# Optimization experiments

Measured on AMD Instinct MI355X. Metric: run time of the kernel, lower is better.

## Reference

```python
import jax, jax.numpy as jnp
import numpy as np

C = 1.0          # ball curvature (Manifold default)
EPS = 1e-7
MIN_NORM = 1e-15

def _artanh(x):
    return jnp.arctanh(jnp.clip(x, -1.0 + EPS, 1.0 - EPS))

def _expmap0(u):
    # exp map at origin of the Poincare ball
    n = jnp.clip(jnp.linalg.norm(u, axis=-1, keepdims=True), MIN_NORM, None)
    sc = np.sqrt(C).astype(np.float32)
    return jnp.tanh(sc * n) * u / (sc * n)

def _mobius_add(x, y):
    x2 = jnp.sum(x * x, axis=-1, keepdims=True)
    y2 = jnp.sum(y * y, axis=-1, keepdims=True)
    xy = jnp.sum(x * y, axis=-1, keepdims=True)
    num = (1.0 + 2.0 * C * xy + C * y2) * x + (1.0 - C * x2) * y
    den = 1.0 + 2.0 * C * xy + C * C * x2 * y2
    return num / jnp.clip(den, MIN_NORM, None)

def setup_inputs() -> dict:
    key = jax.random.key(0)
    k1, k2, k3, k4 = jax.random.split(key, 4)
    N, D, U = 8192, 256, 128
    features = jax.random.normal(k1, (N, D), jnp.float32) * 0.1
    adj = jax.random.randint(k2, (N, N), 0, 2, jnp.int32)
    kernel = jax.random.normal(k3, (D, U), jnp.float32) * (1.0 / np.sqrt(D)).astype(np.float32)
    bias = jax.random.normal(k4, (U,), jnp.float32) * 0.01
    return {"features": features, "adj": adj, "kernel": kernel, "bias": bias}

def reference(features, adj, kernel, bias):
    sc = np.sqrt(C).astype(np.float32)
    # dense matmul then lift to the ball
    x = _expmap0(features @ kernel)                     # [N, U]
    # pairwise hyperbolic distance via closed form of ||mobius_add(-x_i, x_j)||
    x2 = jnp.sum(x * x, axis=-1)                        # [N]
    xy = x @ x.T                                        # [N, N]
    A = 1.0 - 2.0 * C * xy + C * x2[None, :]            # [N, N]
    B = (1.0 - C * x2)[:, None]                         # [N, 1]
    num_sq = A * A * x2[:, None] - 2.0 * A * B * xy + B * B * x2[None, :]
    den = 1.0 - 2.0 * C * xy + C * C * x2[:, None] * x2[None, :]
    mnorm = jnp.sqrt(jnp.clip(num_sq, 0.0, None)) / jnp.clip(den, MIN_NORM, None)
    dist = (2.0 / sc) * _artanh(sc * mnorm)             # sqdist ** 0.5 == distance, [N, N]
    # adjacency-masked softmax (zeros -> -inf, as in tf.where(a != 0, a, float.min))
    a = dist * adj.astype(dist.dtype)
    a = jnp.where(a != 0, a, jnp.finfo(a.dtype).min)
    att = jax.nn.softmax(a, axis=-1)                    # [N, N]
    # mobius_matvec with exchange=True: hyperbolic analogue of att @ x (row-wise norm rescale)
    mx = att @ x                                        # [N, U]
    x_n = jnp.clip(jnp.sqrt(x2)[:, None], MIN_NORM, None)
    mx_n = jnp.clip(jnp.linalg.norm(mx, axis=-1, keepdims=True), MIN_NORM, None)
    out = jnp.tanh(mx_n / x_n * _artanh(sc * x_n)) * mx / (sc * mx_n)
    # hyperbolic bias
    b = _expmap0(bias[None, :])                         # [1, U]
    return _mobius_add(out, b)
```

## Files before the change

### kernel.cpp

```cpp
#include <hip/hip_runtime.h>
#include <hip/hip_bf16.h>
#include <math.h>

#define Nn 8192
#define Dd 256
#define Uu 128
#define MI 16
#define NJC 8
#define JCL (Nn / NJC)
#define NIT (JCL / 16)

typedef __attribute__((ext_vector_type(4))) float f32x4;
typedef __attribute__((ext_vector_type(8))) short s16x8;
typedef __attribute__((ext_vector_type(4))) short s16x4;

#define MFMA_K32(a, b, c) __builtin_amdgcn_mfma_f32_16x16x32_bf16((a), (b), (c), 0, 0, 0)

#define GL_LDS(src, dst)                                                              \
  __builtin_amdgcn_global_load_lds(                                                   \
      (const __attribute__((address_space(1))) unsigned int*)(src),                   \
      (__attribute__((address_space(3))) unsigned int*)(dst), 16, 0, 0)

__device__ __forceinline__ f32x4 mfma_k16(s16x4 a, s16x4 b, f32x4 c){
#if __has_builtin(__builtin_amdgcn_mfma_f32_16x16x16bf16_1k)
  return __builtin_amdgcn_mfma_f32_16x16x16bf16_1k(a, b, c, 0, 0, 0);
#else
  asm("v_mfma_f32_16x16x16_bf16 %0, %1, %2, %0" : "+v"(c) : "v"(a), "v"(b));
  return c;
#endif
}

__device__ __forceinline__ short f2bf(float f){
  unsigned int u = __float_as_uint(f);
  u += 0x7fffu + ((u >> 16) & 1u);
  return (short)(u >> 16);
}

__device__ __forceinline__ float waveSum(float v){
  #pragma unroll
  for (int off = 32; off >= 1; off >>= 1) v += __shfl_xor(v, off);
  return v;
}

__global__ __launch_bounds__(128) void k_prep(const float* __restrict__ feat,
                                              const float* __restrict__ kern,
                                              short* __restrict__ xh,
                                              float* __restrict__ x2){
  const int t = threadIdx.x;
  const int n0 = blockIdx.x * 16;
  __shared__ float fS[16][Dd];
  __shared__ float red[2][16];
  {
    const f32x4* fg = (const f32x4*)(feat + (size_t)n0 * Dd);
    f32x4* fd = (f32x4*)fS;
    #pragma unroll
    for (int c = 0; c < 8; ++c) fd[c * 128 + t] = fg[c * 128 + t];
  }
  __syncthreads();
  float zz[16];
  #pragma unroll
  for (int r = 0; r < 16; ++r) zz[r] = 0.f;
  for (int dq = 0; dq < 64; ++dq){
    const int d = dq * 4;
    const float k0 = kern[(size_t)(d + 0) * Uu + t];
    const float k1 = kern[(size_t)(d + 1) * Uu + t];
    const float k2 = kern[(size_t)(d + 2) * Uu + t];
    const float k3 = kern[(size_t)(d + 3) * Uu + t];
    #pragma unroll
    for (int r = 0; r < 16; ++r){
      const f32x4 f4 = *(const f32x4*)&fS[r][d];
      zz[r] = fmaf(f4.x, k0, fmaf(f4.y, k1, fmaf(f4.z, k2, fmaf(f4.w, k3, zz[r]))));
    }
  }
  #pragma unroll
  for (int r = 0; r < 16; ++r){
    float v = waveSum(zz[r] * zz[r]);
    if ((t & 63) == 0) red[t >> 6][r] = v;
  }
  __syncthreads();
  #pragma unroll
  for (int r = 0; r < 16; ++r){
    const float ns  = red[0][r] + red[1][r];
    const float nrm = fmaxf(sqrtf(ns), 1e-15f);
    const float th  = tanhf(nrm);
    xh[(size_t)(n0 + r) * Uu + t] = f2bf(zz[r] * (th / nrm));
  }
  if (t < 16){
    const float ns  = red[0][t] + red[1][t];
    const float nrm = fmaxf(sqrtf(ns), 1e-15f);
    const float th  = tanhf(nrm);
    x2[n0 + t] = th * th;
  }
}

__global__ __launch_bounds__(256) void k_tr(const short* __restrict__ xh,
                                            short* __restrict__ v3){
  const int n0 = (blockIdx.x & 127) * 64;
  const int u0 = (blockIdx.x >> 7) * 64;
  __shared__ short tS[64][72];
  const int r  = threadIdx.x >> 2;
  const int c0 = (threadIdx.x & 3) * 16;
  const short* src = xh + (size_t)(n0 + r) * Uu + u0 + c0;
  *(s16x8*)&tS[r][c0]     = *(const s16x8*)(src);
  *(s16x8*)&tS[r][c0 + 8] = *(const s16x8*)(src + 8);
  __syncthreads();
  s16x8 b0, b1;
  #pragma unroll
  for (int k = 0; k < 8; ++k){ b0[k] = tS[c0 + k][r]; b1[k] = tS[c0 + 8 + k][r]; }
  short* dst = v3 + (size_t)((n0 + c0) >> 4) * (Uu * 16) + (size_t)(u0 + r) * 16;
  *(s16x8*)(dst)     = b0;
  *(s16x8*)(dst + 8) = b1;
}

__global__ __launch_bounds__(128) void k_bias(const float* __restrict__ bias,
                                              float* __restrict__ bb){
  const int t = threadIdx.x;
  __shared__ float red[2];
  float bv = bias[t];
  float v = waveSum(bv * bv);
  if ((t & 63) == 0) red[t >> 6] = v;
  __syncthreads();
  float n2  = red[0] + red[1];
  float nrm = fmaxf(sqrtf(n2), 1e-15f);
  float th  = tanhf(nrm);
  bb[t] = bv * th / nrm;
  if (t == 0) bb[Uu] = th * th;
}

__global__ __launch_bounds__(256, 4) void k_attn(const int* __restrict__ adj,
                                                 const short* __restrict__ xh,
                                                 const short* __restrict__ v3,
                                                 const float* __restrict__ x2g,
                                                 float* __restrict__ Opart,
                                                 float* __restrict__ lpart){
  const int t    = threadIdx.x;
  const int lane = t & 63;
  const int wid  = t >> 6;
  const int l15  = lane & 15;
  const int q4   = lane >> 4;
  const int ig   = blockIdx.x >> 3;
  const int jc   = blockIdx.x & 7;
  const int i0   = ig * 64 + wid * 16;
  const int irow = i0 + l15;
  const int jbase = jc * JCL;

  __shared__ short kb[2][2048];
  __shared__ short vb[2][2048];

  const char* ksrc = (const char*)xh + (size_t)jbase * 256
                     + (size_t)(lane & 15) * 256 + wid * 64 + (lane >> 4) * 16;
  const char* vsrc = (const char*)v3 + (size_t)jbase * 256 + wid * 1024 + lane * 16;

  GL_LDS(ksrc, (char*)&kb[0][0] + wid * 1024);
  GL_LDS(vsrc, (char*)&vb[0][0] + wid * 1024);

  s16x8 qf[4];
  {
    const short* qp = xh + (size_t)irow * Uu + q4 * 8;
    #pragma unroll
    for (int kk = 0; kk < 4; ++kk) qf[kk] = *(const s16x8*)(qp + kk * 32);
  }
  const float x2i  = x2g[irow];
  const float Bv   = 1.f - x2i;
  const float Bv2j = Bv * Bv;
  const float nBv2 = -2.f * Bv;

  f32x4 oc[8];
  #pragma unroll
  for (int uc = 0; uc < 8; ++uc) oc[uc] = (f32x4){0.f, 0.f, 0.f, 0.f};
  float lacc = 0.f;

  const int itDiag = ((i0 >> 10) == jc) ? ((i0 & 1023) >> 4) : -1;

  const int*   ap  = adj + (size_t)irow * Nn + jbase + q4 * 4;
  const float* x2p = x2g + jbase + q4 * 4;

  int4 aqC = *(const int4*)(ap);
  int4 aqN = *(const int4*)(ap + 16);

  asm volatile("s_waitcnt vmcnt(0)" ::: "memory");
  __builtin_amdgcn_s_barrier();
  __builtin_amdgcn_sched_barrier(0);

  #pragma unroll 1
  for (int it = 0; it < NIT; ++it){
    const int cur = it & 1;
    if (it + 1 < NIT){
      GL_LDS(ksrc + (size_t)(it + 1) * 4096, (char*)&kb[cur ^ 1][0] + wid * 1024);
      GL_LDS(vsrc + (size_t)(it + 1) * 4096, (char*)&vb[cur ^ 1][0] + wid * 1024);
    }
    __builtin_amdgcn_sched_barrier(0);
    const int4 aq2 = *(const int4*)(ap + (((it < NIT - 2) ? (it + 2) : (NIT - 1)) << 4));
    const f32x4 x2j = *(const f32x4*)(x2p + it * 16);

    s16x8 kf[4];
    #pragma unroll
    for (int kk = 0; kk < 4; ++kk)
      kf[kk] = *(const s16x8*)((const char*)&kb[cur][0] + kk * 1024 + lane * 16);
    s16x4 vf[8];
    #pragma unroll
    for (int uc = 0; uc < 8; ++uc)
      vf[uc] = *(const s16x4*)((const char*)&vb[cur][0] + uc * 512 + l15 * 32 + q4 * 8);

    f32x4 s = {0.f, 0.f, 0.f, 0.f};
    s = MFMA_K32(kf[0], qf[0], s);
    s = MFMA_K32(kf[1], qf[1], s);
    s = MFMA_K32(kf[2], qf[2], s);
    s = MFMA_K32(kf[3], qf[3], s);

    const int aarr[4] = {aqC.x, aqC.y, aqC.z, aqC.w};
    const bool dg = (it == itDiag);
    const int j0 = jbase + it * 16;
    s16x4 pb;
    #pragma unroll
    for (int r = 0; r < 4; ++r){
      const float xy  = s[r];
      const float x2v = x2j[r];
      const float Aa  = fmaf(-2.f, xy, 1.f + x2v);
      const float num = fmaf(Aa * Aa, x2i, fmaf(nBv2 * Aa, xy, Bv2j * x2v));
      const float den = fmaf(x2i, x2v, fmaf(-2.f, xy, 1.f));
      const float sq  = sqrtf(fmaxf(num, 0.f));
      const float pd  = fmaxf(den - sq, 1e-30f);
      float p = fminf((den + sq) * __builtin_amdgcn_rcpf(pd), 2.0e7f);
      bool keep = (aarr[r] != 0) && (sq != 0.f);
      if (dg) keep = keep && ((j0 + 4 * q4 + r) != irow);
      p = keep ? p : 0.f;
      lacc += p;
      pb[r] = f2bf(p);
    }

    #pragma unroll
    for (int uc = 0; uc < 8; ++uc) oc[uc] = mfma_k16(vf[uc], pb, oc[uc]);

    aqC = aqN; aqN = aq2;
    asm volatile("s_waitcnt vmcnt(1)" ::: "memory");
    __builtin_amdgcn_s_barrier();
    __builtin_amdgcn_sched_barrier(0);
  }

  lacc += __shfl_xor(lacc, 16);
  lacc += __shfl_xor(lacc, 32);
  if (lane < 16) lpart[(size_t)jc * Nn + i0 + lane] = lacc;
  float* op = Opart + ((size_t)jc * Nn + irow) * Uu + q4 * 4;
  #pragma unroll
  for (int uc = 0; uc < 8; ++uc) *(f32x4*)(op + uc * 16) = oc[uc];
}

__global__ __launch_bounds__(256) void k_out(const float* __restrict__ Opart,
                                             const float* __restrict__ lpart,
                                             const float* __restrict__ x2g,
                                             const float* __restrict__ bb,
                                             float* __restrict__ out){
  const int t  = threadIdx.x;
  const int i0 = blockIdx.x * MI;
  const int er = t >> 4;
  const int ec = t & 15;
  float l = 0.f;
  #pragma unroll
  for (int c = 0; c < NJC; ++c) l += lpart[(size_t)c * Nn + i0 + er];
  const float linv = 1.f / fmaxf(l, 1e-30f);
  float mx[8]; float s2 = 0.f;
  #pragma unroll
  for (int k = 0; k < 8; ++k){
    float v = 0.f;
    #pragma unroll
    for (int c = 0; c < NJC; ++c)
      v += Opart[((size_t)c * Nn + i0 + er) * Uu + ec + 16 * k];
    v *= linv;
    mx[k] = v; s2 = fmaf(v, v, s2);
  }
  s2 += __shfl_xor(s2, 1); s2 += __shfl_xor(s2, 2);
  s2 += __shfl_xor(s2, 4); s2 += __shfl_xor(s2, 8);
  const float mx_n = fmaxf(sqrtf(s2), 1e-15f);
  const float x2e  = x2g[i0 + er];
  const float x_n  = fmaxf(sqrtf(x2e), 1e-15f);
  const float xcl  = fminf(x_n, 1.f - 1e-7f);
  const float art  = 0.5f * __logf((1.f + xcl) / (1.f - xcl));
  const float th   = tanhf(mx_n / x_n * art);
  const float rmn  = th / mx_n;
  float o[8], bu[8]; float ob = 0.f;
  #pragma unroll
  for (int k = 0; k < 8; ++k){
    bu[k] = bb[ec + 16 * k];
    o[k]  = mx[k] * rmn;
    ob = fmaf(o[k], bu[k], ob);
  }
  ob += __shfl_xor(ob, 1); ob += __shfl_xor(ob, 2);
  ob += __shfl_xor(ob, 4); ob += __shfl_xor(ob, 8);
  const float o2   = th * th;
  const float b2   = bb[Uu];
  const float cnum = 1.f + 2.f * ob + b2;
  const float cden = fmaf(o2, b2, 1.f + 2.f * ob);
  const float rden = 1.f / fmaxf(cden, 1e-15f);
  const float co   = 1.f - o2;
  #pragma unroll
  for (int k = 0; k < 8; ++k)
    out[(size_t)(i0 + er) * Uu + ec + 16 * k] = (cnum * o[k] + co * bu[k]) * rden;
}

extern "C" void kernel_launch(void* const* d_in, const int* in_sizes, int n_in,
                              void* d_out, int out_size, void* d_ws, size_t ws_size,
                              hipStream_t stream){
  (void)in_sizes; (void)n_in; (void)out_size; (void)ws_size;
  const float* feat = (const float*)d_in[0];
  const int*   adj  = (const int*)d_in[1];
  const float* kern = (const float*)d_in[2];
  const float* bias = (const float*)d_in[3];

  float* Opart = (float*)d_ws;
  float* lpart = Opart + (size_t)NJC * Nn * Uu;
  float* x2    = lpart + (size_t)NJC * Nn;
  float* bbw   = x2 + Nn;
  short* xh    = (short*)(bbw + 132);
  short* v3    = xh + (size_t)Nn * Uu;

  k_prep<<<Nn / 16, 128, 0, stream>>>(feat, kern, xh, x2);
  k_tr  <<<256, 256, 0, stream>>>(xh, v3);
  k_bias<<<1, 128, 0, stream>>>(bias, bbw);
  k_attn<<<(Nn / 64) * NJC, 256, 0, stream>>>(adj, xh, v3, x2, Opart, lpart);
  k_out <<<Nn / MI, 256, 0, stream>>>(Opart, lpart, x2, bbw, (float*)d_out);
}
```

Measured before the change: 507.3 us.

## Fuse transpose and bias prep into k_prep, stage x2 in LDS, deepen adj prefetch

The prep kernel now also writes the V operand directly in an MFMA-friendly interleaved layout and computes the expmapped bias in block 0. This removes the separate transpose and bias kernels and their launches. The attention kernel loads its whole x2 column slice into LDS once instead of issuing a global load each iteration, uses contiguous per-lane V reads, and prefetches adjacency three iterations ahead instead of two. The trade-off is more registers and extra LDS use, which could reduce occupancy, and layout consistency between the new V packing and the MFMA operand order must be exact.

New measurement: 497.9 us. No clear change (-1.9%).

```diff
diff --git a/kernel.cpp b/kernel.cpp
--- a/kernel.cpp
+++ b/kernel.cpp
@@ -44,12 +44,16 @@
 
 __global__ __launch_bounds__(128) void k_prep(const float* __restrict__ feat,
                                               const float* __restrict__ kern,
+                                              const float* __restrict__ bias,
                                               short* __restrict__ xh,
-                                              float* __restrict__ x2){
+                                              short* __restrict__ v4,
+                                              float* __restrict__ x2,
+                                              float* __restrict__ bb){
   const int t = threadIdx.x;
   const int n0 = blockIdx.x * 16;
   __shared__ float fS[16][Dd];
   __shared__ float red[2][16];
+  __shared__ float redb[2];
   {
     const f32x4* fg = (const f32x4*)(feat + (size_t)n0 * Dd);
     f32x4* fd = (f32x4*)fS;
@@ -78,12 +82,24 @@
     if ((t & 63) == 0) red[t >> 6][r] = v;
   }
   __syncthreads();
+  float scl[16];
   #pragma unroll
   for (int r = 0; r < 16; ++r){
     const float ns  = red[0][r] + red[1][r];
     const float nrm = fmaxf(sqrtf(ns), 1e-15f);
     const float th  = tanhf(nrm);
-    xh[(size_t)(n0 + r) * Uu + t] = f2bf(zz[r] * (th / nrm));
+    scl[r] = th / nrm;
+    xh[(size_t)(n0 + r) * Uu + t] = f2bf(zz[r] * scl[r]);
+  }
+  {
+    short* vt = v4 + (size_t)blockIdx.x * 2048 + (size_t)(t >> 4) * 256 + (t & 15) * 4;
+    #pragma unroll
+    for (int q4w = 0; q4w < 4; ++q4w){
+      s16x4 w;
+      #pragma unroll
+      for (int e = 0; e < 4; ++e) w[e] = f2bf(zz[q4w * 4 + e] * scl[q4w * 4 + e]);
+      *(s16x4*)(vt + q4w * 64) = w;
+    }
   }
   if (t < 16){
     const float ns  = red[0][t] + red[1][t];
@@ -91,45 +107,22 @@
     const float th  = tanhf(nrm);
     x2[n0 + t] = th * th;
   }
-}
-
-__global__ __launch_bounds__(256) void k_tr(const short* __restrict__ xh,
-                                            short* __restrict__ v3){
-  const int n0 = (blockIdx.x & 127) * 64;
-  const int u0 = (blockIdx.x >> 7) * 64;
-  __shared__ short tS[64][72];
-  const int r  = threadIdx.x >> 2;
-  const int c0 = (threadIdx.x & 3) * 16;
-  const short* src = xh + (size_t)(n0 + r) * Uu + u0 + c0;
-  *(s16x8*)&tS[r][c0]     = *(const s16x8*)(src);
-  *(s16x8*)&tS[r][c0 + 8] = *(const s16x8*)(src + 8);
-  __syncthreads();
-  s16x8 b0, b1;
-  #pragma unroll
-  for (int k = 0; k < 8; ++k){ b0[k] = tS[c0 + k][r]; b1[k] = tS[c0 + 8 + k][r]; }
-  short* dst = v3 + (size_t)((n0 + c0) >> 4) * (Uu * 16) + (size_t)(u0 + r) * 16;
-  *(s16x8*)(dst)     = b0;
-  *(s16x8*)(dst + 8) = b1;
-}
-
-__global__ __launch_bounds__(128) void k_bias(const float* __restrict__ bias,
-                                              float* __restrict__ bb){
-  const int t = threadIdx.x;
-  __shared__ float red[2];
-  float bv = bias[t];
-  float v = waveSum(bv * bv);
-  if ((t & 63) == 0) red[t >> 6] = v;
-  __syncthreads();
-  float n2  = red[0] + red[1];
-  float nrm = fmaxf(sqrtf(n2), 1e-15f);
-  float th  = tanhf(nrm);
-  bb[t] = bv * th / nrm;
-  if (t == 0) bb[Uu] = th * th;
+  if (blockIdx.x == 0){
+    const float bv = bias[t];
+    float v = waveSum(bv * bv);
+    if ((t & 63) == 0) redb[t >> 6] = v;
+    __syncthreads();
+    const float n2  = redb[0] + redb[1];
+    const float nrm = fmaxf(sqrtf(n2), 1e-15f);
+    const float th  = tanhf(nrm);
+    bb[t] = bv * th / nrm;
+    if (t == 0) bb[Uu] = th * th;
+  }
 }
 
 __global__ __launch_bounds__(256, 4) void k_attn(const int* __restrict__ adj,
                                                  const short* __restrict__ xh,
-                                                 const short* __restrict__ v3,
+                                                 const short* __restrict__ v4,
                                                  const float* __restrict__ x2g,
                                                  float* __restrict__ Opart,
                                                  float* __restrict__ lpart){
@@ -144,15 +137,17 @@
   const int irow = i0 + l15;
   const int jbase = jc * JCL;
 
-  __shared__ short kb[2][2048];
-  __shared__ short vb[2][2048];
+  __shared__ __align__(16) short kb[2][2048];
+  __shared__ __align__(16) short vb[2][2048];
+  __shared__ __align__(16) float x2S[JCL];
 
   const char* ksrc = (const char*)xh + (size_t)jbase * 256
                      + (size_t)(lane & 15) * 256 + wid * 64 + (lane >> 4) * 16;
-  const char* vsrc = (const char*)v3 + (size_t)jbase * 256 + wid * 1024 + lane * 16;
+  const char* vsrc = (const char*)v4 + (size_t)jbase * 256 + wid * 1024 + lane * 16;
 
   GL_LDS(ksrc, (char*)&kb[0][0] + wid * 1024);
   GL_LDS(vsrc, (char*)&vb[0][0] + wid * 1024);
+  GL_LDS((const char*)(x2g + jbase) + wid * 1024 + lane * 16, (char*)x2S + wid * 1024);
 
   s16x8 qf[4];
   {
@@ -172,11 +167,11 @@
 
   const int itDiag = ((i0 >> 10) == jc) ? ((i0 & 1023) >> 4) : -1;
 
-  const int*   ap  = adj + (size_t)irow * Nn + jbase + q4 * 4;
-  const float* x2p = x2g + jbase + q4 * 4;
-
-  int4 aqC = *(const int4*)(ap);
-  int4 aqN = *(const int4*)(ap + 16);
+  const int* ap = adj + (size_t)irow * Nn + jbase + q4 * 4;
+
+  int4 aqA = *(const int4*)(ap);
+  int4 aqB = *(const int4*)(ap + 16);
+  int4 aqC = *(const int4*)(ap + 32);
 
   asm volatile("s_waitcnt vmcnt(0)" ::: "memory");
   __builtin_amdgcn_s_barrier();
@@ -190,8 +185,7 @@
       GL_LDS(vsrc + (size_t)(it + 1) * 4096, (char*)&vb[cur ^ 1][0] + wid * 1024);
     }
     __builtin_amdgcn_sched_barrier(0);
-    const int4 aq2 = *(const int4*)(ap + (((it < NIT - 2) ? (it + 2) : (NIT - 1)) << 4));
-    const f32x4 x2j = *(const f32x4*)(x2p + it * 16);
+    const int4 aqN = *(const int4*)(ap + (((it + 3 < NIT) ? (it + 3) : (NIT - 1)) << 4));
 
     s16x8 kf[4];
     #pragma unroll
@@ -200,7 +194,8 @@
     s16x4 vf[8];
     #pragma unroll
     for (int uc = 0; uc < 8; ++uc)
-      vf[uc] = *(const s16x4*)((const char*)&vb[cur][0] + uc * 512 + l15 * 32 + q4 * 8);
+      vf[uc] = *(const s16x4*)((const char*)&vb[cur][0] + uc * 512 + lane * 8);
+    const f32x4 x2j = *(const f32x4*)&x2S[it * 16 + q4 * 4];
 
     f32x4 s = {0.f, 0.f, 0.f, 0.f};
     s = MFMA_K32(kf[0], qf[0], s);
@@ -208,7 +203,7 @@
     s = MFMA_K32(kf[2], qf[2], s);
     s = MFMA_K32(kf[3], qf[3], s);
 
-    const int aarr[4] = {aqC.x, aqC.y, aqC.z, aqC.w};
+    const int aarr[4] = {aqA.x, aqA.y, aqA.z, aqA.w};
     const bool dg = (it == itDiag);
     const int j0 = jbase + it * 16;
     s16x4 pb;
@@ -232,7 +227,7 @@
     #pragma unroll
     for (int uc = 0; uc < 8; ++uc) oc[uc] = mfma_k16(vf[uc], pb, oc[uc]);
 
-    aqC = aqN; aqN = aq2;
+    aqA = aqB; aqB = aqC; aqC = aqN;
     asm volatile("s_waitcnt vmcnt(1)" ::: "memory");
     __builtin_amdgcn_s_barrier();
     __builtin_amdgcn_sched_barrier(0);
@@ -312,11 +307,9 @@
   float* x2    = lpart + (size_t)NJC * Nn;
   float* bbw   = x2 + Nn;
   short* xh    = (short*)(bbw + 132);
-  short* v3    = xh + (size_t)Nn * Uu;
-
-  k_prep<<<Nn / 16, 128, 0, stream>>>(feat, kern, xh, x2);
-  k_tr  <<<256, 256, 0, stream>>>(xh, v3);
-  k_bias<<<1, 128, 0, stream>>>(bias, bbw);
-  k_attn<<<(Nn / 64) * NJC, 256, 0, stream>>>(adj, xh, v3, x2, Opart, lpart);
+  short* v4    = xh + (size_t)Nn * Uu;
+
+  k_prep<<<Nn / 16, 128, 0, stream>>>(feat, kern, bias, xh, v4, x2, bbw);
+  k_attn<<<(Nn / 64) * NJC, 256, 0, stream>>>(adj, xh, v4, x2, Opart, lpart);
   k_out <<<Nn / MI, 256, 0, stream>>>(Opart, lpart, x2, bbw, (float*)d_out);
 }
```
